# Kernel optimization log

Measured on AMD Instinct MI355X. Metric: run time of the kernel, lower is better.

## Reference

```python
import jax, jax.numpy as jnp
import numpy as np
import math

N = 8192
DIM = 256

def setup_inputs() -> dict:
    key = jax.random.key(0)
    k1, k2, k3 = jax.random.split(key, 3)
    h = jax.random.normal(k1, (N, DIM), dtype=jnp.float32)
    # xavier_uniform with gain=1.414 for square [dim, dim] matrices
    gain = 1.414
    bound = gain * math.sqrt(6.0 / (DIM + DIM))
    Wq = jax.random.uniform(k2, (DIM, DIM), dtype=jnp.float32, minval=-bound, maxval=bound)
    Wk = jax.random.uniform(k3, (DIM, DIM), dtype=jnp.float32, minval=-bound, maxval=bound)
    return {"h": h, "Wq": Wq, "Wk": Wk}

def reference(h, Wq, Wk):
    dim = h.shape[1]
    q = h @ Wq                                   # [N, dim]
    k = h @ Wk                                   # [N, dim]
    e = (q @ k.T) / jnp.sqrt(jnp.asarray(dim, h.dtype))  # [N, N]
    attention = jax.nn.softmax(e, axis=1)        # row-wise softmax
    attention = attention.mean(axis=0)           # [N], column-mean over rows
    x = attention @ h                            # [dim]
    return x
```

## Files before the change

### kernel.cpp

```cpp
#include <hip/hip_runtime.h>
#include <cstdint>
#include <cstddef>


#define N_ROWS 8192
#define DIM    256

typedef __bf16 bf16x8 __attribute__((ext_vector_type(8)));
typedef unsigned short u16x8 __attribute__((ext_vector_type(8)));
typedef float f32x16 __attribute__((ext_vector_type(16)));

__device__ __forceinline__ uint16_t f2bf(float f) {
    uint32_t u = __float_as_uint(f);
    uint32_t r = (u + 0x7fffu + ((u >> 16) & 1u)) >> 16;
    return (uint16_t)r;
}

__device__ __forceinline__ void gld16(const void* gsrc, void* ldst) {
    __builtin_amdgcn_global_load_lds(
        (const __attribute__((address_space(1))) unsigned int*)gsrc,
        (__attribute__((address_space(3))) unsigned int*)ldst, 16, 0, 0);
}

__device__ __forceinline__ size_t frag_off(int i, int d) {
    int tile = i >> 5, il = i & 31;
    int a0 = d >> 4, hi = (d >> 3) & 1, j = d & 7;
    return (size_t)tile * 8192 + (size_t)((a0 * 64) + il + 32 * hi) * 8 + j;
}

__global__ __launch_bounds__(256) void proj_kernel(
        const float* __restrict__ h, const float* __restrict__ Wq,
        const float* __restrict__ Wk, uint16_t* __restrict__ qf,
        uint16_t* __restrict__ kf, float* __restrict__ l_arr,
        float* __restrict__ c_arr, float* __restrict__ out) {
    __shared__ alignas(16) uint16_t wb[256 * 128];
    const int tid = threadIdx.x, lane = tid & 63, wave = tid >> 6;
    const int which = blockIdx.x & 1;
    const int rt = blockIdx.x >> 1;

    if (blockIdx.x < 32)       l_arr[blockIdx.x * 256 + tid] = 0.0f;
    else if (blockIdx.x < 64)  c_arr[(blockIdx.x - 32) * 256 + tid] = 0.0f;
    else if (blockIdx.x == 64) out[tid] = 0.0f;

    const float* __restrict__ W = which ? Wk : Wq;
    uint16_t* __restrict__ dst = which ? kf : qf;
    const float scale = which ? 1.0f : 0.0625f;

    bf16x8 afrag[16];
    {
        const int r = rt * 32 + (lane & 31);
        const float* hp = h + (size_t)r * DIM + ((lane >> 5) * 8);
#pragma unroll
        for (int a0 = 0; a0 < 16; a0++) {
            float4 f0 = *(const float4*)(hp + a0 * 16);
            float4 f1 = *(const float4*)(hp + a0 * 16 + 4);
            u16x8 f;
            f[0] = f2bf(f0.x); f[1] = f2bf(f0.y); f[2] = f2bf(f0.z); f[3] = f2bf(f0.w);
            f[4] = f2bf(f1.x); f[5] = f2bf(f1.y); f[6] = f2bf(f1.z); f[7] = f2bf(f1.w);
            afrag[a0] = __builtin_bit_cast(bf16x8, f);
        }
    }

    for (int p = 0; p < 2; p++) {
        __syncthreads();
#pragma unroll
        for (int c = 0; c < 32; c++) {
            int f = c * 256 + tid;
            int k = f >> 5, nc = (f & 31) * 4;
            float4 w4 = *(const float4*)&W[(size_t)k * DIM + p * 128 + nc];
            ushort4 b;
            b.x = f2bf(w4.x); b.y = f2bf(w4.y); b.z = f2bf(w4.z); b.w = f2bf(w4.w);
            *(ushort4*)&wb[k * 128 + nc] = b;
        }
        __syncthreads();

        const int ct = wave;
        f32x16 acc;
#pragma unroll
        for (int i = 0; i < 16; i++) acc[i] = 0.0f;
        const int cl = ct * 32 + (lane & 31);
#pragma unroll
        for (int a0 = 0; a0 < 16; a0++) {
            const int kb = a0 * 16 + (lane >> 5) * 8;
            u16x8 f;
#pragma unroll
            for (int j = 0; j < 8; j++) f[j] = wb[(kb + j) * 128 + cl];
            acc = __builtin_amdgcn_mfma_f32_32x32x16_bf16(
                afrag[a0], __builtin_bit_cast(bf16x8, f), acc, 0, 0, 0);
        }
        const int dcol = p * 128 + ct * 32 + (lane & 31);
        const int rb0 = rt * 32 + 4 * (lane >> 5);
#pragma unroll
        for (int reg = 0; reg < 16; reg++) {
            int row = rb0 + (reg & 3) + 8 * (reg >> 2);
            dst[frag_off(row, dcol)] = f2bf(acc[reg] * scale);
        }
    }
}

template <int MODE>
__global__ __launch_bounds__(256, 3) void pass_kernel(
        const uint16_t* __restrict__ qf, const uint16_t* __restrict__ kf,
        float* __restrict__ l_arr, float* __restrict__ c_arr) {
    __shared__ alignas(16) uint16_t ktile[2][8192];
    __shared__ float c_lds[512];
    const int tid = threadIdx.x, lane = tid & 63, wave = tid >> 6;
    const int bid = blockIdx.x;
    const int cc = (bid & 7) | (((bid >> 3) & 1) << 3);
    const int rb = bid >> 4;
    const int t0 = rb * 4 + wave;

    bf16x8 qreg[16];
    {
        const uint4* qp = (const uint4*)qf;
#pragma unroll
        for (int a0 = 0; a0 < 16; a0++)
            qreg[a0] = __builtin_bit_cast(bf16x8, qp[(size_t)t0 * 1024 + a0 * 64 + lane]);
    }

    float rs[16];
    float rr[16];
    if (MODE == 0) {
#pragma unroll
        for (int reg = 0; reg < 16; reg++) rs[reg] = 0.0f;
    } else {
#pragma unroll
        for (int reg = 0; reg < 16; reg++) {
            int row = rb * 128 + wave * 32 + (reg & 3) + 8 * (reg >> 2) + 4 * (lane >> 5);
            rr[reg] = 1.0f / (8192.0f * l_arr[row]);
        }
        for (int i = tid; i < 512; i += 256) c_lds[i] = 0.0f;
    }

    const char* ksrc = (const char*)(kf + (size_t)cc * 16 * 8192);

    {
        const char* s0 = ksrc + wave * 4096 + lane * 16;
        char* d0 = (char*)&ktile[0][0] + wave * 4096;
#pragma unroll
        for (int it = 0; it < 4; it++) gld16(s0 + it * 1024, d0 + it * 1024);
    }

    f32x16 ae, ao;
#pragma unroll
    for (int i = 0; i < 16; i++) { ae[i] = 0.0f; ao[i] = 0.0f; }

    for (int step = 0; step < 16; step++) {
        __syncthreads();
        if (step < 15) {
            const char* sn = ksrc + (step + 1) * 16384 + wave * 4096 + lane * 16;
            char* dn = (char*)&ktile[(step + 1) & 1][0] + wave * 4096;
#pragma unroll
            for (int it = 0; it < 4; it++) gld16(sn + it * 1024, dn + it * 1024);
        }

        if (step > 0) {
            if (MODE == 0) {
#pragma unroll
                for (int reg = 0; reg < 16; reg++) rs[reg] += __expf(ae[reg] + ao[reg]);
            } else {
                float s = 0.0f;
#pragma unroll
                for (int reg = 0; reg < 16; reg++) s += __expf(ae[reg] + ao[reg]) * rr[reg];
                s += __shfl_xor(s, 32);
                if (lane < 32) atomicAdd(&c_lds[(step - 1) * 32 + lane], s);
            }
#pragma unroll
            for (int i = 0; i < 16; i++) { ae[i] = 0.0f; ao[i] = 0.0f; }
        }

        const uint16_t* kt = &ktile[step & 1][0];
#pragma unroll
        for (int a0 = 0; a0 < 8; a0++) {
            bf16x8 b0 = __builtin_bit_cast(bf16x8,
                *(const u16x8*)&kt[(size_t)((2 * a0) * 64 + lane) * 8]);
            bf16x8 b1 = __builtin_bit_cast(bf16x8,
                *(const u16x8*)&kt[(size_t)((2 * a0 + 1) * 64 + lane) * 8]);
            ae = __builtin_amdgcn_mfma_f32_32x32x16_bf16(qreg[2 * a0], b0, ae, 0, 0, 0);
            ao = __builtin_amdgcn_mfma_f32_32x32x16_bf16(qreg[2 * a0 + 1], b1, ao, 0, 0, 0);
        }
    }

    if (MODE == 0) {
#pragma unroll
        for (int reg = 0; reg < 16; reg++) rs[reg] += __expf(ae[reg] + ao[reg]);
#pragma unroll
        for (int reg = 0; reg < 16; reg++) {
            float v = rs[reg];
            v += __shfl_xor(v, 1);  v += __shfl_xor(v, 2);  v += __shfl_xor(v, 4);
            v += __shfl_xor(v, 8);  v += __shfl_xor(v, 16);
            if ((lane & 31) == 0) {
                int row = rb * 128 + wave * 32 + (reg & 3) + 8 * (reg >> 2) + 4 * (lane >> 5);
                atomicAdd(&l_arr[row], v);
            }
        }
    } else {
        float s = 0.0f;
#pragma unroll
        for (int reg = 0; reg < 16; reg++) s += __expf(ae[reg] + ao[reg]) * rr[reg];
        s += __shfl_xor(s, 32);
        if (lane < 32) atomicAdd(&c_lds[15 * 32 + lane], s);
        __syncthreads();
        for (int i = tid; i < 512; i += 256) atomicAdd(&c_arr[cc * 512 + i], c_lds[i]);
    }
}

__global__ __launch_bounds__(256) void finish_kernel(
        const float* __restrict__ h, const float* __restrict__ c_arr,
        float* __restrict__ out) {
    const int d = threadIdx.x;
    const int j0 = blockIdx.x * 64;
    float acc = 0.0f;
    for (int j = j0; j < j0 + 64; j++) acc += c_arr[j] * h[(size_t)j * DIM + d];
    atomicAdd(&out[d], acc);
}

extern "C" void kernel_launch(void* const* d_in, const int* in_sizes, int n_in,
                              void* d_out, int out_size, void* d_ws, size_t ws_size,
                              hipStream_t stream) {
    const float* h  = (const float*)d_in[0];
    const float* Wq = (const float*)d_in[1];
    const float* Wk = (const float*)d_in[2];

    uint16_t* qf = (uint16_t*)d_ws;
    uint16_t* kf = qf + (size_t)N_ROWS * DIM;
    float* l_arr = (float*)((char*)d_ws + (size_t)8 * 1024 * 1024);
    float* c_arr = l_arr + N_ROWS;
    float* out = (float*)d_out;

    proj_kernel<<<512, 256, 0, stream>>>(h, Wq, Wk, qf, kf, l_arr, c_arr, out);
    pass_kernel<0><<<1024, 256, 0, stream>>>(qf, kf, l_arr, c_arr);
    pass_kernel<1><<<1024, 256, 0, stream>>>(qf, kf, l_arr, c_arr);
    finish_kernel<<<128, 256, 0, stream>>>(h, c_arr, out);
}
```

Baseline: 180.3 us.

## Load K fragments directly to registers, process two Q tiles per wave

The pass kernels stop staging K tiles in LDS through async global-to-LDS loads. Each wave now streams K fragments straight from global memory into registers with register double-buffering, and reuses each K fragment across two 32-row Q tiles, so the grid is halved. The projection kernel writes its fragment-layout output through an LDS staging buffer, giving coalesced 16-byte stores in place of scattered 2-byte writes. The cost is higher register pressure (two Q fragment sets and two accumulators, launch bounds lowered to 2 blocks per SIMD) and reliance on L2 for K reuse across waves.

```diff
diff --git a/kernel.cpp b/kernel.cpp
--- a/kernel.cpp
+++ b/kernel.cpp
@@ -14,18 +14,6 @@
     uint32_t u = __float_as_uint(f);
     uint32_t r = (u + 0x7fffu + ((u >> 16) & 1u)) >> 16;
     return (uint16_t)r;
-}
-
-__device__ __forceinline__ void gld16(const void* gsrc, void* ldst) {
-    __builtin_amdgcn_global_load_lds(
-        (const __attribute__((address_space(1))) unsigned int*)gsrc,
-        (__attribute__((address_space(3))) unsigned int*)ldst, 16, 0, 0);
-}
-
-__device__ __forceinline__ size_t frag_off(int i, int d) {
-    int tile = i >> 5, il = i & 31;
-    int a0 = d >> 4, hi = (d >> 3) & 1, j = d & 7;
-    return (size_t)tile * 8192 + (size_t)((a0 * 64) + il + 32 * hi) * 8 + j;
 }
 
 __global__ __launch_bounds__(256) void proj_kernel(
@@ -34,6 +22,7 @@
         uint16_t* __restrict__ kf, float* __restrict__ l_arr,
         float* __restrict__ c_arr, float* __restrict__ out) {
     __shared__ alignas(16) uint16_t wb[256 * 128];
+    __shared__ alignas(16) uint16_t rep[4][2048];
     const int tid = threadIdx.x, lane = tid & 63, wave = tid >> 6;
     const int which = blockIdx.x & 1;
     const int rt = blockIdx.x >> 1;
@@ -74,11 +63,10 @@
         }
         __syncthreads();
 
-        const int ct = wave;
         f32x16 acc;
 #pragma unroll
         for (int i = 0; i < 16; i++) acc[i] = 0.0f;
-        const int cl = ct * 32 + (lane & 31);
+        const int cl = wave * 32 + (lane & 31);
 #pragma unroll
         for (int a0 = 0; a0 < 16; a0++) {
             const int kb = a0 * 16 + (lane >> 5) * 8;
@@ -88,118 +76,133 @@
             acc = __builtin_amdgcn_mfma_f32_32x32x16_bf16(
                 afrag[a0], __builtin_bit_cast(bf16x8, f), acc, 0, 0, 0);
         }
-        const int dcol = p * 128 + ct * 32 + (lane & 31);
-        const int rb0 = rt * 32 + 4 * (lane >> 5);
-#pragma unroll
-        for (int reg = 0; reg < 16; reg++) {
-            int row = rb0 + (reg & 3) + 8 * (reg >> 2);
-            dst[frag_off(row, dcol)] = f2bf(acc[reg] * scale);
+
+        {
+            const int dcl = lane & 31;
+            const int a0o = dcl >> 4, hi = (dcl >> 3) & 1, j = dcl & 7;
+            const int ilb = 4 * (lane >> 5);
+#pragma unroll
+            for (int reg = 0; reg < 16; reg++) {
+                int il = ilb + (reg & 3) + 8 * (reg >> 2);
+                rep[wave][(size_t)((a0o * 64) + il + 32 * hi) * 8 + j] =
+                    f2bf(acc[reg] * scale);
+            }
+            const uint4* rp = (const uint4*)&rep[wave][0];
+            uint4* gp = (uint4*)(dst + (size_t)rt * 8192 +
+                                 (size_t)(p * 8 + wave * 2) * 512);
+            gp[lane * 2]     = rp[lane * 2];
+            gp[lane * 2 + 1] = rp[lane * 2 + 1];
         }
     }
 }
 
 template <int MODE>
-__global__ __launch_bounds__(256, 3) void pass_kernel(
+__global__ __launch_bounds__(256, 2) void qk_pass(
         const uint16_t* __restrict__ qf, const uint16_t* __restrict__ kf,
         float* __restrict__ l_arr, float* __restrict__ c_arr) {
-    __shared__ alignas(16) uint16_t ktile[2][8192];
     __shared__ float c_lds[512];
     const int tid = threadIdx.x, lane = tid & 63, wave = tid >> 6;
     const int bid = blockIdx.x;
-    const int cc = (bid & 7) | (((bid >> 3) & 1) << 3);
+    const int cc = ((bid & 7) << 1) | ((bid >> 3) & 1);
     const int rb = bid >> 4;
-    const int t0 = rb * 4 + wave;
-
-    bf16x8 qreg[16];
+    const int t0 = rb * 8 + wave * 2;
+
+    const uint4* qp = (const uint4*)qf;
+    bf16x8 q0[16], q1[16];
+#pragma unroll
+    for (int a0 = 0; a0 < 16; a0++) {
+        q0[a0] = __builtin_bit_cast(bf16x8, qp[(size_t)t0 * 1024 + a0 * 64 + lane]);
+        q1[a0] = __builtin_bit_cast(bf16x8, qp[(size_t)(t0 + 1) * 1024 + a0 * 64 + lane]);
+    }
+
+    float rs0[16], rs1[16];
+    float rr0[16], rr1[16];
+    if (MODE == 0) {
+#pragma unroll
+        for (int r = 0; r < 16; r++) { rs0[r] = 0.0f; rs1[r] = 0.0f; }
+    } else {
+#pragma unroll
+        for (int r = 0; r < 16; r++) {
+            int ro = (r & 3) + 8 * (r >> 2) + 4 * (lane >> 5);
+            rr0[r] = 1.0f / (8192.0f * l_arr[t0 * 32 + ro]);
+            rr1[r] = 1.0f / (8192.0f * l_arr[(t0 + 1) * 32 + ro]);
+        }
+        for (int i = tid; i < 512; i += 256) c_lds[i] = 0.0f;
+        __syncthreads();
+    }
+
+    const uint4* kp = (const uint4*)kf;
+    bf16x8 b[2][4];
     {
-        const uint4* qp = (const uint4*)qf;
-#pragma unroll
-        for (int a0 = 0; a0 < 16; a0++)
-            qreg[a0] = __builtin_bit_cast(bf16x8, qp[(size_t)t0 * 1024 + a0 * 64 + lane]);
-    }
-
-    float rs[16];
-    float rr[16];
+        const uint4* kt = kp + (size_t)(cc * 16) * 1024;
+#pragma unroll
+        for (int i = 0; i < 4; i++)
+            b[0][i] = __builtin_bit_cast(bf16x8, kt[i * 64 + lane]);
+    }
+
+    f32x16 acc0, acc1;
+#pragma unroll
+    for (int i = 0; i < 16; i++) { acc0[i] = 0.0f; acc1[i] = 0.0f; }
+
+    for (int s = 0; s < 16; s++) {
+        const uint4* kt  = kp + (size_t)(cc * 16 + s) * 1024;
+        const uint4* ktn = kt + 1024;
+#pragma unroll
+        for (int qd = 0; qd < 4; qd++) {
+            const int cur = qd & 1, nxt = cur ^ 1;
+            if (qd < 3) {
+#pragma unroll
+                for (int i = 0; i < 4; i++)
+                    b[nxt][i] = __builtin_bit_cast(bf16x8,
+                        kt[((qd + 1) * 4 + i) * 64 + lane]);
+            } else if (s < 15) {
+#pragma unroll
+                for (int i = 0; i < 4; i++)
+                    b[nxt][i] = __builtin_bit_cast(bf16x8, ktn[i * 64 + lane]);
+            }
+#pragma unroll
+            for (int i = 0; i < 4; i++) {
+                acc0 = __builtin_amdgcn_mfma_f32_32x32x16_bf16(
+                    q0[qd * 4 + i], b[cur][i], acc0, 0, 0, 0);
+                acc1 = __builtin_amdgcn_mfma_f32_32x32x16_bf16(
+                    q1[qd * 4 + i], b[cur][i], acc1, 0, 0, 0);
+            }
+        }
+        if (MODE == 0) {
+#pragma unroll
+            for (int r = 0; r < 16; r++) {
+                rs0[r] += __expf(acc0[r]);  acc0[r] = 0.0f;
+                rs1[r] += __expf(acc1[r]);  acc1[r] = 0.0f;
+            }
+        } else {
+            float sv = 0.0f;
+#pragma unroll
+            for (int r = 0; r < 16; r++) {
+                sv += __expf(acc0[r]) * rr0[r];  acc0[r] = 0.0f;
+                sv += __expf(acc1[r]) * rr1[r];  acc1[r] = 0.0f;
+            }
+            sv += __shfl_xor(sv, 32);
+            if (lane < 32) atomicAdd(&c_lds[s * 32 + lane], sv);
+        }
+    }
+
     if (MODE == 0) {
 #pragma unroll
-        for (int reg = 0; reg < 16; reg++) rs[reg] = 0.0f;
+        for (int r = 0; r < 16; r++) {
+            int ro = (r & 3) + 8 * (r >> 2) + 4 * (lane >> 5);
+            float v0 = rs0[r], v1 = rs1[r];
+            v0 += __shfl_xor(v0, 1);  v0 += __shfl_xor(v0, 2);
+            v0 += __shfl_xor(v0, 4);  v0 += __shfl_xor(v0, 8);
+            v0 += __shfl_xor(v0, 16);
+            v1 += __shfl_xor(v1, 1);  v1 += __shfl_xor(v1, 2);
+            v1 += __shfl_xor(v1, 4);  v1 += __shfl_xor(v1, 8);
+            v1 += __shfl_xor(v1, 16);
+            if ((lane & 31) == 0) {
+                atomicAdd(&l_arr[t0 * 32 + ro], v0);
+                atomicAdd(&l_arr[(t0 + 1) * 32 + ro], v1);
+            }
+        }
     } else {
-#pragma unroll
-        for (int reg = 0; reg < 16; reg++) {
-            int row = rb * 128 + wave * 32 + (reg & 3) + 8 * (reg >> 2) + 4 * (lane >> 5);
-            rr[reg] = 1.0f / (8192.0f * l_arr[row]);
-        }
-        for (int i = tid; i < 512; i += 256) c_lds[i] = 0.0f;
-    }
-
-    const char* ksrc = (const char*)(kf + (size_t)cc * 16 * 8192);
-
-    {
-        const char* s0 = ksrc + wave * 4096 + lane * 16;
-        char* d0 = (char*)&ktile[0][0] + wave * 4096;
-#pragma unroll
-        for (int it = 0; it < 4; it++) gld16(s0 + it * 1024, d0 + it * 1024);
-    }
-
-    f32x16 ae, ao;
-#pragma unroll
-    for (int i = 0; i < 16; i++) { ae[i] = 0.0f; ao[i] = 0.0f; }
-
-    for (int step = 0; step < 16; step++) {
-        __syncthreads();
-        if (step < 15) {
-            const char* sn = ksrc + (step + 1) * 16384 + wave * 4096 + lane * 16;
-            char* dn = (char*)&ktile[(step + 1) & 1][0] + wave * 4096;
-#pragma unroll
-            for (int it = 0; it < 4; it++) gld16(sn + it * 1024, dn + it * 1024);
-        }
-
-        if (step > 0) {
-            if (MODE == 0) {
-#pragma unroll
-                for (int reg = 0; reg < 16; reg++) rs[reg] += __expf(ae[reg] + ao[reg]);
-            } else {
-                float s = 0.0f;
-#pragma unroll
-                for (int reg = 0; reg < 16; reg++) s += __expf(ae[reg] + ao[reg]) * rr[reg];
-                s += __shfl_xor(s, 32);
-                if (lane < 32) atomicAdd(&c_lds[(step - 1) * 32 + lane], s);
-            }
-#pragma unroll
-            for (int i = 0; i < 16; i++) { ae[i] = 0.0f; ao[i] = 0.0f; }
-        }
-
-        const uint16_t* kt = &ktile[step & 1][0];
-#pragma unroll
-        for (int a0 = 0; a0 < 8; a0++) {
-            bf16x8 b0 = __builtin_bit_cast(bf16x8,
-                *(const u16x8*)&kt[(size_t)((2 * a0) * 64 + lane) * 8]);
-            bf16x8 b1 = __builtin_bit_cast(bf16x8,
-                *(const u16x8*)&kt[(size_t)((2 * a0 + 1) * 64 + lane) * 8]);
-            ae = __builtin_amdgcn_mfma_f32_32x32x16_bf16(qreg[2 * a0], b0, ae, 0, 0, 0);
-            ao = __builtin_amdgcn_mfma_f32_32x32x16_bf16(qreg[2 * a0 + 1], b1, ao, 0, 0, 0);
-        }
-    }
-
-    if (MODE == 0) {
-#pragma unroll
-        for (int reg = 0; reg < 16; reg++) rs[reg] += __expf(ae[reg] + ao[reg]);
-#pragma unroll
-        for (int reg = 0; reg < 16; reg++) {
-            float v = rs[reg];
-            v += __shfl_xor(v, 1);  v += __shfl_xor(v, 2);  v += __shfl_xor(v, 4);
-            v += __shfl_xor(v, 8);  v += __shfl_xor(v, 16);
-            if ((lane & 31) == 0) {
-                int row = rb * 128 + wave * 32 + (reg & 3) + 8 * (reg >> 2) + 4 * (lane >> 5);
-                atomicAdd(&l_arr[row], v);
-            }
-        }
-    } else {
-        float s = 0.0f;
-#pragma unroll
-        for (int reg = 0; reg < 16; reg++) s += __expf(ae[reg] + ao[reg]) * rr[reg];
-        s += __shfl_xor(s, 32);
-        if (lane < 32) atomicAdd(&c_lds[15 * 32 + lane], s);
         __syncthreads();
         for (int i = tid; i < 512; i += 256) atomicAdd(&c_arr[cc * 512 + i], c_lds[i]);
     }
@@ -229,7 +232,7 @@
     float* out = (float*)d_out;
 
     proj_kernel<<<512, 256, 0, stream>>>(h, Wq, Wk, qf, kf, l_arr, c_arr, out);
-    pass_kernel<0><<<1024, 256, 0, stream>>>(qf, kf, l_arr, c_arr);
-    pass_kernel<1><<<1024, 256, 0, stream>>>(qf, kf, l_arr, c_arr);
+    qk_pass<0><<<512, 256, 0, stream>>>(qf, kf, l_arr, c_arr);
+    qk_pass<1><<<512, 256, 0, stream>>>(qf, kf, l_arr, c_arr);
     finish_kernel<<<128, 256, 0, stream>>>(h, c_arr, out);
 }
```

Result: no change. 182.1 us (+1.0%).
